# Performance work log

Hardware: AMD Instinct MI355X
Metric: run time of the kernel (lower is better)

## Reference

```python
import jax, jax.numpy as jnp
import numpy as np

SAMPLE_RATE = 2048.0
FFTLENGTH = 8.0
NUM_BINS = 16
FFTSIZE = int(FFTLENGTH * SAMPLE_RATE)          # 16384
NUM_FREQS = FFTSIZE // 2 + 1                    # 8193
DF = 1.0 / FFTLENGTH                            # frequency resolution


def setup_inputs() -> dict:
    key = jax.random.key(0)
    k1, k2 = jax.random.split(key)
    template = jax.random.normal(k1, (512, 2, FFTSIZE), dtype=jnp.float32)
    strain = jax.random.normal(k2, (512, 2, FFTSIZE), dtype=jnp.float32)
    return {"template": template, "strain": strain}


def _snr_series(htilde, stilde):
    # snr_frequency_series with psd=None (pre-whitened strain):
    # 4 * df * Re(conj(h) * s)
    return 4.0 * DF * (jnp.conj(htilde) * stilde).real


def reference(template, strain):
    # time -> frequency domain
    htilde = jnp.fft.rfft(template, axis=-1) / SAMPLE_RATE   # [B,C,F] c64
    stilde = jnp.fft.rfft(strain, axis=-1) / SAMPLE_RATE

    # partition_frequencies: cumulative optimal SNR of the template
    cum_h = jnp.cumsum(_snr_series(htilde, htilde), axis=-1)  # [B,C,F]
    total_h = cum_h[..., -1:]                                 # [B,C,1]
    bins = (jnp.arange(NUM_BINS + 1, dtype=cum_h.dtype) / NUM_BINS) * total_h
    # per-row searchsorted (side='right'), vmapped over batch and channel
    edges = jax.vmap(jax.vmap(
        lambda a, v: jnp.searchsorted(a, v, side='right')))(cum_h, bins)
    edges = jnp.clip(edges, 0, cum_h.shape[-1] - 1)           # [B,C,NB+1]
    qtilde = htilde / jnp.sqrt(total_h)                       # normalized template

    # get_snr_per_bin: cumulative matched-filter SNR, gathered at bin edges
    cum_q = jnp.cumsum(_snr_series(qtilde, stilde), axis=-1)  # [B,C,F]
    right = jnp.take_along_axis(cum_q, edges[..., 1:], axis=-1)
    left = jnp.take_along_axis(cum_q, edges[..., :-1], axis=-1)
    snr_per_bin = right - left                                # [B,C,NB]
    total_snr = cum_q[..., -1:]                               # [B,C,1]

    chisq_summand = (snr_per_bin - total_snr / NUM_BINS) ** 2
    chisq = chisq_summand.sum(axis=-1) * (NUM_BINS / (NUM_BINS - 1))
    return chisq                                              # [B,C]
```

## Files before the change

### kernel.cpp

```cpp
#include <hip/hip_runtime.h>
#include <math.h>

#define DPI 3.14159265358979323846

__device__ __forceinline__ float2 cmul(float2 a, float2 b) {
    return make_float2(a.x*b.x - a.y*b.y, a.x*b.y + a.y*b.x);
}
__device__ __forceinline__ float2 cadd(float2 a, float2 b){ return make_float2(a.x+b.x, a.y+b.y); }
__device__ __forceinline__ float2 csub(float2 a, float2 b){ return make_float2(a.x-b.x, a.y-b.y); }

__device__ const float TW32R[16] = {
    1.0f, 0.98078528040323045f, 0.92387953251128676f, 0.83146961230254524f,
    0.70710678118654752f, 0.55557023301960222f, 0.38268343236508977f, 0.19509032201612827f,
    0.0f, -0.19509032201612827f, -0.38268343236508977f, -0.55557023301960222f,
    -0.70710678118654752f, -0.83146961230254524f, -0.92387953251128676f, -0.98078528040323045f };
__device__ const float TW32I[16] = {
    0.0f, -0.19509032201612827f, -0.38268343236508977f, -0.55557023301960222f,
    -0.70710678118654752f, -0.83146961230254524f, -0.92387953251128676f, -0.98078528040323045f,
    -1.0f, -0.98078528040323045f, -0.92387953251128676f, -0.83146961230254524f,
    -0.70710678118654752f, -0.55557023301960222f, -0.38268343236508977f, -0.19509032201612827f };

__device__ const int BR4[16] = {0,8,4,12,2,10,6,14,1,9,5,13,3,11,7,15};

template<int H>
__device__ __forceinline__ void stage16(float2* y) {
    #pragma unroll
    for (int g = 0; g < 16; g += 2*H) {
        #pragma unroll
        for (int j = 0; j < H; j++) {
            float2 u = y[g+j], v = y[g+j+H];
            y[g+j] = cadd(u, v);
            float2 d = csub(u, v);
            const int m = j * (16 / H);
            y[g+j+H] = (j == 0) ? d : cmul(d, make_float2(TW32R[m], TW32I[m]));
        }
    }
}
__device__ __forceinline__ void fft16(float2* y) {
    stage16<8>(y); stage16<4>(y); stage16<2>(y); stage16<1>(y);
}

__device__ __forceinline__ void pow16(float2 w, float2* wp) {
    wp[0] = make_float2(1.f, 0.f);
    wp[1] = w;
    wp[2] = cmul(w, w);
    wp[3] = cmul(wp[2], w);
    wp[4] = cmul(wp[2], wp[2]);
    wp[5] = cmul(wp[4], wp[1]);
    wp[6] = cmul(wp[4], wp[2]);
    wp[7] = cmul(wp[4], wp[3]);
    wp[8] = cmul(wp[4], wp[4]);
    wp[9] = cmul(wp[8], wp[1]);
    wp[10] = cmul(wp[8], wp[2]);
    wp[11] = cmul(wp[8], wp[3]);
    wp[12] = cmul(wp[8], wp[4]);
    wp[13] = cmul(wp[8], wp[5]);
    wp[14] = cmul(wp[8], wp[6]);
    wp[15] = cmul(wp[8], wp[7]);
}

static __global__ void init_tw(float2* __restrict__ ws) {
    int g = blockIdx.x * 1024 + threadIdx.x;
    if (g < 512) {
        ws[g] = make_float2((float)cos(DPI*g/4096.0), (float)(-sin(DPI*g/4096.0)));
    } else if (g < 544) {
        int j = g - 512;
        ws[g] = make_float2((float)cos(DPI*j/256.0), (float)(-sin(DPI*j/256.0)));
    } else if (g < 1568) {
        int q = g - 544;
        ws[g] = make_float2((float)cos(DPI*q/1024.0), (float)(-sin(DPI*q/1024.0)));
    } else if (g < 1576) {
        int i = g - 1568;
        ws[g] = make_float2((float)cos(DPI*i/8192.0), (float)(-sin(DPI*i/8192.0)));
    }
}

__launch_bounds__(1024, 4)
static __global__ void chisq_kernel(const float* __restrict__ tmpl,
                                    const float* __restrict__ strn,
                                    const float2* __restrict__ ws,
                                    float* __restrict__ out)
{
    __shared__ float2 Z[16384];
    float* F = reinterpret_cast<float*>(Z);
    int*   I = reinterpret_cast<int*>(Z);

    const int t    = threadIdx.x;
    const int half = t >> 9;
    const int u    = t & 511;
    const int row  = blockIdx.x;
    const float ALPHA = 1.1920928955078125e-7f;

    const float2* tw8192 = ws;
    const float2* tw512  = ws + 512;
    const float2* twC    = ws + 544;
    const float2* twI    = ws + 1568;

    float2* Zh = Z + (half << 13);
    const float* src = (half ? tmpl : strn) + (size_t)row * 16384;

    {
        const float2* x = reinterpret_cast<const float2*>(src);
        float2 y[16];

        #pragma unroll
        for (int n1 = 0; n1 < 16; n1++) y[n1] = x[n1*512 + u];
        fft16(y);
        {
            float2 wp[16]; pow16(tw8192[u], wp);
            #pragma unroll
            for (int p = 0; p < 16; p++) {
                int k1 = BR4[p];
                float2 val = y[p];
                if (k1 > 0) val = cmul(val, wp[k1]);
                Zh[(u << 4) | (k1 ^ (u & 15))] = val;
            }
        }
        __syncthreads();

        const int k1s = u >> 5, js = u & 31;
        #pragma unroll
        for (int n2 = 0; n2 < 16; n2++)
            y[n2] = Zh[((n2*32 + js) << 4) | (k1s ^ (js & 15))];
        __syncthreads();
        fft16(y);
        {
            float2 wq[16]; pow16(tw512[js], wq);
            #pragma unroll
            for (int p = 0; p < 16; p++) {
                int k2 = BR4[p];
                float2 val = y[p];
                if (k2 > 0) val = cmul(val, wq[k2]);
                Zh[(k1s << 9) + (k2 << 5) + (js ^ k2)] = val;
            }
        }
        __syncthreads();

        const int f = u >> 8, k1t = (u >> 4) & 15, k2t = u & 15;
        const int base = (k1t << 9) + (k2t << 5);
        if (f == 0) {
            #pragma unroll
            for (int j2 = 0; j2 < 16; j2++) {
                float2 a = Zh[base + (j2 ^ k2t)];
                float2 b = Zh[base + (j2 ^ k2t) + 16];
                y[j2] = cadd(a, b);
            }
        } else {
            #pragma unroll
            for (int j2 = 0; j2 < 16; j2++) {
                float2 a = Zh[base + (j2 ^ k2t)];
                float2 b = Zh[base + (j2 ^ k2t) + 16];
                y[j2] = cmul(csub(a, b), make_float2(TW32R[j2], TW32I[j2]));
            }
        }
        __syncthreads();
        fft16(y);
        #pragma unroll
        for (int p = 0; p < 16; p++) {
            int s2 = BR4[p];
            int k = k1t + (k2t << 4) + (f << 8) + (s2 << 9);
            Zh[(k & ~31) | ((k & 31) ^ ((k >> 5) & 31))] = y[p];
        }
        __syncthreads();
    }

    float2* ZS = Z;
    float2* ZH = Z + 8192;
    float2 zs0 = ZS[0], zh0 = ZH[0];
    const float s_nyq = zs0.x - zs0.y;
    const float h_nyq = zh0.x - zh0.y;

    float hh[8], hs[8];
    {
        float2 cv = twC[t];
        #pragma unroll
        for (int i = 0; i < 8; i++) {
            int k = (t << 3) + i;
            int m = (8192 - k) & 8191;
            int ak = (k & ~31) | ((k & 31) ^ ((k >> 5) & 31));
            int am = (m & ~31) | ((m & 31) ^ ((m >> 5) & 31));
            float2 As = ZS[ak], Bs = ZS[am];
            float2 Ah = ZH[ak], Bh = ZH[am];
            float2 w = cmul(cv, twI[i]);
            float Er = 0.5f*(As.x + Bs.x), Ei = 0.5f*(As.y - Bs.y);
            float Dr = 0.5f*(As.x - Bs.x), Di = 0.5f*(As.y + Bs.y);
            float sr = Er + w.x*Di + w.y*Dr;
            float si = Ei + w.y*Di - w.x*Dr;
            Er = 0.5f*(Ah.x + Bh.x); Ei = 0.5f*(Ah.y - Bh.y);
            Dr = 0.5f*(Ah.x - Bh.x); Di = 0.5f*(Ah.y + Bh.y);
            float hr = Er + w.x*Di + w.y*Dr;
            float hi = Ei + w.y*Di - w.x*Dr;
            hh[i] = hr*hr + hi*hi;
            hs[i] = hr*sr + hi*si;
        }
    }
    __syncthreads();

    const int SCANW = 16500;
    const int EDG   = 16520;
    const int BINS  = 16544;
    const int TOT   = 16561;

    float run = 0.f;
    #pragma unroll
    for (int i = 0; i < 8; i++) run += ALPHA * hh[i];

    const int lane = t & 63, wid = t >> 6;
    float v = run;
    #pragma unroll
    for (int off = 1; off < 64; off <<= 1) {
        float o = __shfl_up(v, off, 64);
        if (lane >= off) v += o;
    }
    if (lane == 63) F[SCANW + wid] = v;
    __syncthreads();
    float wbase = 0.f;
    #pragma unroll
    for (int w2 = 0; w2 < 15; w2++) if (w2 < wid) wbase += F[SCANW + w2];
    float base = wbase + v - run;

    float cum = base;
    #pragma unroll
    for (int i = 0; i < 8; i++) {
        cum += ALPHA * hh[i];
        int k = (t << 3) + i;
        F[k + (k >> 5)] = cum;
    }
    if (t == 1023) F[8448] = cum + ALPHA * h_nyq * h_nyq;
    __syncthreads();

    float total_h = F[8448];
    if (t < 17) {
        float target = (float)t * 0.0625f * total_h;
        int lo = 0, hi = 8193;
        while (lo < hi) {
            int mid = (lo + hi) >> 1;
            float vv = F[mid + (mid >> 5)];
            if (vv <= target) lo = mid + 1; else hi = mid;
        }
        I[EDG + t] = lo < 8192 ? lo : 8192;
    }
    if (t >= 64 && t < 80) F[BINS + (t - 64)] = 0.f;
    if (t == 80) F[TOT] = 0.f;
    __syncthreads();

    int e[17];
    #pragma unroll
    for (int i = 0; i < 17; i++) e[i] = I[EDG + i];

    float invs = 1.0f / sqrtf(total_h);
    float qs   = ALPHA * invs;

    float tot = 0.f, acc = 0.f;
    int   cur = -1;
    #pragma unroll
    for (int i = 0; i < 8; i++) {
        int   k = (t << 3) + i;
        float r = qs * hs[i];
        tot += r;
        int bn = -1;
        #pragma unroll
        for (int j = 0; j < 17; j++) bn += (e[j] < k) ? 1 : 0;
        if (bn != cur) {
            if (cur >= 0) atomicAdd(&F[BINS + cur], acc);
            acc = 0.f;
            cur = bn;
        }
        acc += r;
    }
    if (cur >= 0) atomicAdd(&F[BINS + cur], acc);

    #pragma unroll
    for (int off = 32; off > 0; off >>= 1) tot += __shfl_down(tot, off);
    if ((t & 63) == 0) atomicAdd(&F[TOT], tot);

    if (t == 0) {
        float rn = qs * (h_nyq * s_nyq);
        atomicAdd(&F[TOT], rn);
        int bn = -1;
        #pragma unroll
        for (int j = 0; j < 17; j++) bn += (e[j] < 8192) ? 1 : 0;
        if (bn >= 0) atomicAdd(&F[BINS + bn], rn);
    }
    __syncthreads();

    if (t == 0) {
        float total = F[TOT];
        float mean  = total * 0.0625f;
        float chisq = 0.f;
        #pragma unroll
        for (int j = 0; j < 16; j++) {
            float d = F[BINS + j] - mean;
            chisq += d * d;
        }
        out[row] = chisq * (16.0f / 15.0f);
    }
}

extern "C" void kernel_launch(void* const* d_in, const int* in_sizes, int n_in,
                              void* d_out, int out_size, void* d_ws, size_t ws_size,
                              hipStream_t stream) {
    const float* tmpl = (const float*)d_in[0];
    const float* strn = (const float*)d_in[1];
    float* outp = (float*)d_out;
    float2* ws  = (float2*)d_ws;

    int rows = in_sizes[0] / 16384;

    hipLaunchKernelGGL(init_tw, dim3(2), dim3(1024), 0, stream, ws);
    hipLaunchKernelGGL(chisq_kernel, dim3(rows), dim3(1024), 0, stream,
                       tmpl, strn, ws, outp);
}
```

Before: 81.79 us.

## Process several rows per block and prefetch next row's input during FFT

Each block now handles RPB=4 rows in a loop instead of one row per block. The next row's global loads are issued into registers right after the first FFT pass, so they can overlap with the remaining FFT stages and the chi-square reduction of the current row. The cost is fewer blocks in the grid (rows/4, which for 1024 rows is 256 blocks, about the CU count), which reduces parallelism across CUs. It also raises register pressure from the held prefetch buffer.

```diff
diff --git a/kernel.cpp b/kernel.cpp
--- a/kernel.cpp
+++ b/kernel.cpp
@@ -2,6 +2,7 @@
 #include <math.h>
 
 #define DPI 3.14159265358979323846
+#define RPB 4
 
 __device__ __forceinline__ float2 cmul(float2 a, float2 b) {
     return make_float2(a.x*b.x - a.y*b.y, a.x*b.y + a.y*b.x);
@@ -79,7 +80,8 @@
 static __global__ void chisq_kernel(const float* __restrict__ tmpl,
                                     const float* __restrict__ strn,
                                     const float2* __restrict__ ws,
-                                    float* __restrict__ out)
+                                    float* __restrict__ out,
+                                    int rows)
 {
     __shared__ float2 Z[16384];
     float* F = reinterpret_cast<float*>(Z);
@@ -88,7 +90,6 @@
     const int t    = threadIdx.x;
     const int half = t >> 9;
     const int u    = t & 511;
-    const int row  = blockIdx.x;
     const float ALPHA = 1.1920928955078125e-7f;
 
     const float2* tw8192 = ws;
@@ -97,26 +98,43 @@
     const float2* twI    = ws + 1568;
 
     float2* Zh = Z + (half << 13);
-    const float* src = (half ? tmpl : strn) + (size_t)row * 16384;
-
-    {
-        const float2* x = reinterpret_cast<const float2*>(src);
-        float2 y[16];
-
-        #pragma unroll
-        for (int n1 = 0; n1 < 16; n1++) y[n1] = x[n1*512 + u];
-        fft16(y);
+    const float* sig = half ? tmpl : strn;
+    const float2 cv = twC[t];
+
+    const int r0 = blockIdx.x * RPB;
+
+    float2 P[16];
+    if (r0 < rows) {
+        const float2* x = reinterpret_cast<const float2*>(sig + (size_t)r0 * 16384);
+        #pragma unroll
+        for (int n1 = 0; n1 < 16; n1++) P[n1] = x[n1*512 + u];
+    }
+
+    for (int rr = 0; rr < RPB; rr++) {
+        const int row = r0 + rr;
+        if (row >= rows) break;
+
+        fft16(P);
+        __syncthreads();
         {
             float2 wp[16]; pow16(tw8192[u], wp);
             #pragma unroll
             for (int p = 0; p < 16; p++) {
                 int k1 = BR4[p];
-                float2 val = y[p];
+                float2 val = P[p];
                 if (k1 > 0) val = cmul(val, wp[k1]);
                 Zh[(u << 4) | (k1 ^ (u & 15))] = val;
             }
         }
-        __syncthreads();
+
+        if (rr + 1 < RPB && row + 1 < rows) {
+            const float2* xn = reinterpret_cast<const float2*>(sig + (size_t)(row + 1) * 16384);
+            #pragma unroll
+            for (int n1 = 0; n1 < 16; n1++) P[n1] = xn[n1*512 + u];
+        }
+        __syncthreads();
+
+        float2 y[16];
 
         const int k1s = u >> 5, js = u & 31;
         #pragma unroll
@@ -162,17 +180,14 @@
             Zh[(k & ~31) | ((k & 31) ^ ((k >> 5) & 31))] = y[p];
         }
         __syncthreads();
-    }
-
-    float2* ZS = Z;
-    float2* ZH = Z + 8192;
-    float2 zs0 = ZS[0], zh0 = ZH[0];
-    const float s_nyq = zs0.x - zs0.y;
-    const float h_nyq = zh0.x - zh0.y;
-
-    float hh[8], hs[8];
-    {
-        float2 cv = twC[t];
+
+        float2* ZS = Z;
+        float2* ZH = Z + 8192;
+        float2 zs0 = ZS[0], zh0 = ZH[0];
+        const float s_nyq = zs0.x - zs0.y;
+        const float h_nyq = zh0.x - zh0.y;
+
+        float hh[8], hs[8];
         #pragma unroll
         for (int i = 0; i < 8; i++) {
             int k = (t << 3) + i;
@@ -193,107 +208,107 @@
             hh[i] = hr*hr + hi*hi;
             hs[i] = hr*sr + hi*si;
         }
-    }
-    __syncthreads();
-
-    const int SCANW = 16500;
-    const int EDG   = 16520;
-    const int BINS  = 16544;
-    const int TOT   = 16561;
-
-    float run = 0.f;
-    #pragma unroll
-    for (int i = 0; i < 8; i++) run += ALPHA * hh[i];
-
-    const int lane = t & 63, wid = t >> 6;
-    float v = run;
-    #pragma unroll
-    for (int off = 1; off < 64; off <<= 1) {
-        float o = __shfl_up(v, off, 64);
-        if (lane >= off) v += o;
-    }
-    if (lane == 63) F[SCANW + wid] = v;
-    __syncthreads();
-    float wbase = 0.f;
-    #pragma unroll
-    for (int w2 = 0; w2 < 15; w2++) if (w2 < wid) wbase += F[SCANW + w2];
-    float base = wbase + v - run;
-
-    float cum = base;
-    #pragma unroll
-    for (int i = 0; i < 8; i++) {
-        cum += ALPHA * hh[i];
-        int k = (t << 3) + i;
-        F[k + (k >> 5)] = cum;
-    }
-    if (t == 1023) F[8448] = cum + ALPHA * h_nyq * h_nyq;
-    __syncthreads();
-
-    float total_h = F[8448];
-    if (t < 17) {
-        float target = (float)t * 0.0625f * total_h;
-        int lo = 0, hi = 8193;
-        while (lo < hi) {
-            int mid = (lo + hi) >> 1;
-            float vv = F[mid + (mid >> 5)];
-            if (vv <= target) lo = mid + 1; else hi = mid;
-        }
-        I[EDG + t] = lo < 8192 ? lo : 8192;
-    }
-    if (t >= 64 && t < 80) F[BINS + (t - 64)] = 0.f;
-    if (t == 80) F[TOT] = 0.f;
-    __syncthreads();
-
-    int e[17];
-    #pragma unroll
-    for (int i = 0; i < 17; i++) e[i] = I[EDG + i];
-
-    float invs = 1.0f / sqrtf(total_h);
-    float qs   = ALPHA * invs;
-
-    float tot = 0.f, acc = 0.f;
-    int   cur = -1;
-    #pragma unroll
-    for (int i = 0; i < 8; i++) {
-        int   k = (t << 3) + i;
-        float r = qs * hs[i];
-        tot += r;
-        int bn = -1;
-        #pragma unroll
-        for (int j = 0; j < 17; j++) bn += (e[j] < k) ? 1 : 0;
-        if (bn != cur) {
-            if (cur >= 0) atomicAdd(&F[BINS + cur], acc);
-            acc = 0.f;
-            cur = bn;
-        }
-        acc += r;
-    }
-    if (cur >= 0) atomicAdd(&F[BINS + cur], acc);
-
-    #pragma unroll
-    for (int off = 32; off > 0; off >>= 1) tot += __shfl_down(tot, off);
-    if ((t & 63) == 0) atomicAdd(&F[TOT], tot);
-
-    if (t == 0) {
-        float rn = qs * (h_nyq * s_nyq);
-        atomicAdd(&F[TOT], rn);
-        int bn = -1;
-        #pragma unroll
-        for (int j = 0; j < 17; j++) bn += (e[j] < 8192) ? 1 : 0;
-        if (bn >= 0) atomicAdd(&F[BINS + bn], rn);
-    }
-    __syncthreads();
-
-    if (t == 0) {
-        float total = F[TOT];
-        float mean  = total * 0.0625f;
-        float chisq = 0.f;
-        #pragma unroll
-        for (int j = 0; j < 16; j++) {
-            float d = F[BINS + j] - mean;
-            chisq += d * d;
-        }
-        out[row] = chisq * (16.0f / 15.0f);
+        __syncthreads();
+
+        const int SCANW = 16500;
+        const int EDG   = 16520;
+        const int BINS  = 16544;
+        const int TOT   = 16561;
+
+        float run = 0.f;
+        #pragma unroll
+        for (int i = 0; i < 8; i++) run += ALPHA * hh[i];
+
+        const int lane = t & 63, wid = t >> 6;
+        float v = run;
+        #pragma unroll
+        for (int off = 1; off < 64; off <<= 1) {
+            float o = __shfl_up(v, off, 64);
+            if (lane >= off) v += o;
+        }
+        if (lane == 63) F[SCANW + wid] = v;
+        __syncthreads();
+        float wbase = 0.f;
+        #pragma unroll
+        for (int w2 = 0; w2 < 15; w2++) if (w2 < wid) wbase += F[SCANW + w2];
+        float base2 = wbase + v - run;
+
+        float cum = base2;
+        #pragma unroll
+        for (int i = 0; i < 8; i++) {
+            cum += ALPHA * hh[i];
+            int k = (t << 3) + i;
+            F[k + (k >> 5)] = cum;
+        }
+        if (t == 1023) F[8448] = cum + ALPHA * h_nyq * h_nyq;
+        __syncthreads();
+
+        float total_h = F[8448];
+        if (t < 17) {
+            float target = (float)t * 0.0625f * total_h;
+            int lo = 0, hi = 8193;
+            while (lo < hi) {
+                int mid = (lo + hi) >> 1;
+                float vv = F[mid + (mid >> 5)];
+                if (vv <= target) lo = mid + 1; else hi = mid;
+            }
+            I[EDG + t] = lo < 8192 ? lo : 8192;
+        }
+        if (t >= 64 && t < 80) F[BINS + (t - 64)] = 0.f;
+        if (t == 80) F[TOT] = 0.f;
+        __syncthreads();
+
+        int e[17];
+        #pragma unroll
+        for (int i = 0; i < 17; i++) e[i] = I[EDG + i];
+
+        float invs = 1.0f / sqrtf(total_h);
+        float qs   = ALPHA * invs;
+
+        float tot = 0.f, acc = 0.f;
+        int   cur = -1;
+        #pragma unroll
+        for (int i = 0; i < 8; i++) {
+            int   k = (t << 3) + i;
+            float r = qs * hs[i];
+            tot += r;
+            int bn = -1;
+            #pragma unroll
+            for (int j = 0; j < 17; j++) bn += (e[j] < k) ? 1 : 0;
+            if (bn != cur) {
+                if (cur >= 0) atomicAdd(&F[BINS + cur], acc);
+                acc = 0.f;
+                cur = bn;
+            }
+            acc += r;
+        }
+        if (cur >= 0) atomicAdd(&F[BINS + cur], acc);
+
+        #pragma unroll
+        for (int off = 32; off > 0; off >>= 1) tot += __shfl_down(tot, off);
+        if ((t & 63) == 0) atomicAdd(&F[TOT], tot);
+
+        if (t == 0) {
+            float rn = qs * (h_nyq * s_nyq);
+            atomicAdd(&F[TOT], rn);
+            int bn = -1;
+            #pragma unroll
+            for (int j = 0; j < 17; j++) bn += (e[j] < 8192) ? 1 : 0;
+            if (bn >= 0) atomicAdd(&F[BINS + bn], rn);
+        }
+        __syncthreads();
+
+        if (t == 0) {
+            float total = F[TOT];
+            float mean  = total * 0.0625f;
+            float chisq = 0.f;
+            #pragma unroll
+            for (int j = 0; j < 16; j++) {
+                float d = F[BINS + j] - mean;
+                chisq += d * d;
+            }
+            out[row] = chisq * (16.0f / 15.0f);
+        }
     }
 }
 
@@ -306,8 +321,9 @@
     float2* ws  = (float2*)d_ws;
 
     int rows = in_sizes[0] / 16384;
+    int nblk = (rows + RPB - 1) / RPB;
 
     hipLaunchKernelGGL(init_tw, dim3(2), dim3(1024), 0, stream, ws);
-    hipLaunchKernelGGL(chisq_kernel, dim3(rows), dim3(1024), 0, stream,
-                       tmpl, strn, ws, outp);
-}
+    hipLaunchKernelGGL(chisq_kernel, dim3(nblk), dim3(1024), 0, stream,
+                       tmpl, strn, ws, outp, rows);
+}
```

After: 187.3 us. +129.0%, slower.

## Run strain and template FFTs sequentially in 512-thread blocks with half LDS

Applied to the files above, without the earlier changes.

Each block now uses 512 threads and a single 64 KB shared buffer, performing the strain FFT first, saving its unpacked real-FFT bins in registers, then reusing the same LDS for the template FFT. Halving LDS per block is meant to let more blocks reside per CU and improve latency hiding. The cost is serialising the two FFTs within a block, and doubling per-thread register state (16 bins each for strain and template), which may limit occupancy.

```diff
diff --git a/kernel.cpp b/kernel.cpp
--- a/kernel.cpp
+++ b/kernel.cpp
@@ -66,62 +66,57 @@
     } else if (g < 544) {
         int j = g - 512;
         ws[g] = make_float2((float)cos(DPI*j/256.0), (float)(-sin(DPI*j/256.0)));
-    } else if (g < 1568) {
+    } else if (g < 1056) {
         int q = g - 544;
-        ws[g] = make_float2((float)cos(DPI*q/1024.0), (float)(-sin(DPI*q/1024.0)));
-    } else if (g < 1576) {
-        int i = g - 1568;
+        ws[g] = make_float2((float)cos(DPI*q/512.0), (float)(-sin(DPI*q/512.0)));
+    } else if (g < 1072) {
+        int i = g - 1056;
         ws[g] = make_float2((float)cos(DPI*i/8192.0), (float)(-sin(DPI*i/8192.0)));
     }
 }
 
-__launch_bounds__(1024, 4)
+__launch_bounds__(512, 2)
 static __global__ void chisq_kernel(const float* __restrict__ tmpl,
                                     const float* __restrict__ strn,
                                     const float2* __restrict__ ws,
                                     float* __restrict__ out)
 {
-    __shared__ float2 Z[16384];
+    __shared__ float2 Z[8192];
     float* F = reinterpret_cast<float*>(Z);
     int*   I = reinterpret_cast<int*>(Z);
 
-    const int t    = threadIdx.x;
-    const int half = t >> 9;
-    const int u    = t & 511;
-    const int row  = blockIdx.x;
+    const int t   = threadIdx.x;
+    const int row = blockIdx.x;
     const float ALPHA = 1.1920928955078125e-7f;
 
     const float2* tw8192 = ws;
     const float2* tw512  = ws + 512;
-    const float2* twC    = ws + 544;
-    const float2* twI    = ws + 1568;
-
-    float2* Zh = Z + (half << 13);
-    const float* src = (half ? tmpl : strn) + (size_t)row * 16384;
-
-    {
-        const float2* x = reinterpret_cast<const float2*>(src);
+    const float2* twB    = ws + 544;
+    const float2* twI    = ws + 1056;
+
+    const int k1s = t >> 5, js = t & 31;
+    const int f = t >> 8, k1t = (t >> 4) & 15, k2t = t & 15;
+
+    auto run_fft = [&](const float* srcrow) {
         float2 y[16];
-
-        #pragma unroll
-        for (int n1 = 0; n1 < 16; n1++) y[n1] = x[n1*512 + u];
+        const float2* x = reinterpret_cast<const float2*>(srcrow);
+        #pragma unroll
+        for (int n1 = 0; n1 < 16; n1++) y[n1] = x[n1*512 + t];
         fft16(y);
         {
-            float2 wp[16]; pow16(tw8192[u], wp);
+            float2 wp[16]; pow16(tw8192[t], wp);
             #pragma unroll
             for (int p = 0; p < 16; p++) {
                 int k1 = BR4[p];
                 float2 val = y[p];
                 if (k1 > 0) val = cmul(val, wp[k1]);
-                Zh[(u << 4) | (k1 ^ (u & 15))] = val;
+                Z[(t << 4) | (k1 ^ (t & 15))] = val;
             }
         }
         __syncthreads();
-
-        const int k1s = u >> 5, js = u & 31;
         #pragma unroll
         for (int n2 = 0; n2 < 16; n2++)
-            y[n2] = Zh[((n2*32 + js) << 4) | (k1s ^ (js & 15))];
+            y[n2] = Z[((n2*32 + js) << 4) | (k1s ^ (js & 15))];
         __syncthreads();
         fft16(y);
         {
@@ -131,25 +126,23 @@
                 int k2 = BR4[p];
                 float2 val = y[p];
                 if (k2 > 0) val = cmul(val, wq[k2]);
-                Zh[(k1s << 9) + (k2 << 5) + (js ^ k2)] = val;
+                Z[(k1s << 9) + (k2 << 5) + (js ^ k2)] = val;
             }
         }
         __syncthreads();
-
-        const int f = u >> 8, k1t = (u >> 4) & 15, k2t = u & 15;
         const int base = (k1t << 9) + (k2t << 5);
         if (f == 0) {
             #pragma unroll
             for (int j2 = 0; j2 < 16; j2++) {
-                float2 a = Zh[base + (j2 ^ k2t)];
-                float2 b = Zh[base + (j2 ^ k2t) + 16];
+                float2 a = Z[base + (j2 ^ k2t)];
+                float2 b = Z[base + (j2 ^ k2t) + 16];
                 y[j2] = cadd(a, b);
             }
         } else {
             #pragma unroll
             for (int j2 = 0; j2 < 16; j2++) {
-                float2 a = Zh[base + (j2 ^ k2t)];
-                float2 b = Zh[base + (j2 ^ k2t) + 16];
+                float2 a = Z[base + (j2 ^ k2t)];
+                float2 b = Z[base + (j2 ^ k2t) + 16];
                 y[j2] = cmul(csub(a, b), make_float2(TW32R[j2], TW32I[j2]));
             }
         }
@@ -159,51 +152,67 @@
         for (int p = 0; p < 16; p++) {
             int s2 = BR4[p];
             int k = k1t + (k2t << 4) + (f << 8) + (s2 << 9);
-            Zh[(k & ~31) | ((k & 31) ^ ((k >> 5) & 31))] = y[p];
-        }
-        __syncthreads();
-    }
-
-    float2* ZS = Z;
-    float2* ZH = Z + 8192;
-    float2 zs0 = ZS[0], zh0 = ZH[0];
-    const float s_nyq = zs0.x - zs0.y;
-    const float h_nyq = zh0.x - zh0.y;
-
-    float hh[8], hs[8];
+            Z[(k & ~31) | ((k & 31) ^ ((k >> 5) & 31))] = y[p];
+        }
+        __syncthreads();
+    };
+
+    float sre[16], sim[16];
+    float s_nyq;
+    run_fft(strn + (size_t)row * 16384);
     {
-        float2 cv = twC[t];
-        #pragma unroll
-        for (int i = 0; i < 8; i++) {
-            int k = (t << 3) + i;
+        const float2 cv = twB[t];
+        #pragma unroll
+        for (int i = 0; i < 16; i++) {
+            int k = (t << 4) + i;
             int m = (8192 - k) & 8191;
             int ak = (k & ~31) | ((k & 31) ^ ((k >> 5) & 31));
             int am = (m & ~31) | ((m & 31) ^ ((m >> 5) & 31));
-            float2 As = ZS[ak], Bs = ZS[am];
-            float2 Ah = ZH[ak], Bh = ZH[am];
+            float2 A = Z[ak], B = Z[am];
             float2 w = cmul(cv, twI[i]);
-            float Er = 0.5f*(As.x + Bs.x), Ei = 0.5f*(As.y - Bs.y);
-            float Dr = 0.5f*(As.x - Bs.x), Di = 0.5f*(As.y + Bs.y);
-            float sr = Er + w.x*Di + w.y*Dr;
-            float si = Ei + w.y*Di - w.x*Dr;
-            Er = 0.5f*(Ah.x + Bh.x); Ei = 0.5f*(Ah.y - Bh.y);
-            Dr = 0.5f*(Ah.x - Bh.x); Di = 0.5f*(Ah.y + Bh.y);
+            float Er = 0.5f*(A.x + B.x), Ei = 0.5f*(A.y - B.y);
+            float Dr = 0.5f*(A.x - B.x), Di = 0.5f*(A.y + B.y);
+            sre[i] = Er + w.x*Di + w.y*Dr;
+            sim[i] = Ei + w.y*Di - w.x*Dr;
+        }
+        float2 z0 = Z[0];
+        s_nyq = z0.x - z0.y;
+    }
+    __syncthreads();
+
+    float hh[16], hs[16];
+    float h_nyq;
+    run_fft(tmpl + (size_t)row * 16384);
+    {
+        const float2 cv = twB[t];
+        #pragma unroll
+        for (int i = 0; i < 16; i++) {
+            int k = (t << 4) + i;
+            int m = (8192 - k) & 8191;
+            int ak = (k & ~31) | ((k & 31) ^ ((k >> 5) & 31));
+            int am = (m & ~31) | ((m & 31) ^ ((m >> 5) & 31));
+            float2 A = Z[ak], B = Z[am];
+            float2 w = cmul(cv, twI[i]);
+            float Er = 0.5f*(A.x + B.x), Ei = 0.5f*(A.y - B.y);
+            float Dr = 0.5f*(A.x - B.x), Di = 0.5f*(A.y + B.y);
             float hr = Er + w.x*Di + w.y*Dr;
             float hi = Ei + w.y*Di - w.x*Dr;
             hh[i] = hr*hr + hi*hi;
-            hs[i] = hr*sr + hi*si;
-        }
-    }
-    __syncthreads();
-
-    const int SCANW = 16500;
-    const int EDG   = 16520;
-    const int BINS  = 16544;
-    const int TOT   = 16561;
+            hs[i] = hr*sre[i] + hi*sim[i];
+        }
+        float2 z0 = Z[0];
+        h_nyq = z0.x - z0.y;
+    }
+    __syncthreads();
+
+    const int SCANW = 8456;
+    const int EDG   = 8466;
+    const int BINS  = 8484;
+    const int TOT   = 8501;
 
     float run = 0.f;
     #pragma unroll
-    for (int i = 0; i < 8; i++) run += ALPHA * hh[i];
+    for (int i = 0; i < 16; i++) run += ALPHA * hh[i];
 
     const int lane = t & 63, wid = t >> 6;
     float v = run;
@@ -216,17 +225,17 @@
     __syncthreads();
     float wbase = 0.f;
     #pragma unroll
-    for (int w2 = 0; w2 < 15; w2++) if (w2 < wid) wbase += F[SCANW + w2];
-    float base = wbase + v - run;
-
-    float cum = base;
-    #pragma unroll
-    for (int i = 0; i < 8; i++) {
+    for (int w2 = 0; w2 < 7; w2++) if (w2 < wid) wbase += F[SCANW + w2];
+    float base2 = wbase + v - run;
+
+    float cum = base2;
+    #pragma unroll
+    for (int i = 0; i < 16; i++) {
         cum += ALPHA * hh[i];
-        int k = (t << 3) + i;
+        int k = (t << 4) + i;
         F[k + (k >> 5)] = cum;
     }
-    if (t == 1023) F[8448] = cum + ALPHA * h_nyq * h_nyq;
+    if (t == 511) F[8448] = cum + ALPHA * h_nyq * h_nyq;
     __syncthreads();
 
     float total_h = F[8448];
@@ -254,8 +263,8 @@
     float tot = 0.f, acc = 0.f;
     int   cur = -1;
     #pragma unroll
-    for (int i = 0; i < 8; i++) {
-        int   k = (t << 3) + i;
+    for (int i = 0; i < 16; i++) {
+        int   k = (t << 4) + i;
         float r = qs * hs[i];
         tot += r;
         int bn = -1;
@@ -308,6 +317,6 @@
     int rows = in_sizes[0] / 16384;
 
     hipLaunchKernelGGL(init_tw, dim3(2), dim3(1024), 0, stream, ws);
-    hipLaunchKernelGGL(chisq_kernel, dim3(rows), dim3(1024), 0, stream,
+    hipLaunchKernelGGL(chisq_kernel, dim3(rows), dim3(512), 0, stream,
                        tmpl, strn, ws, outp);
 }
```

Result: slower. 91.24 us (+11.5%).
